# Performance work log

Hardware: AMD Instinct MI355X
Metric: run time of the kernel (lower is better)

## Reference

```python
import jax, jax.numpy as jnp
import numpy as np

B, N, HIDDEN = 1024, 64, 1152
NUM_CLASSES = 1000
OUT_DIM = 4 * 4 * 8  # patch_size^2 * out_channels = 128


def setup_inputs() -> dict:
    key = jax.random.key(0)
    k_x, k_y, k_w = jax.random.split(key, 3)
    x = jax.random.normal(k_x, (B, N, HIDDEN), dtype=jnp.float32)
    y = jax.random.randint(k_y, (B,), 0, NUM_CLASSES, dtype=jnp.int64)
    weight = 0.02 * jax.random.normal(k_w, (NUM_CLASSES, HIDDEN, OUT_DIM), dtype=jnp.float32)
    bias = jnp.zeros((NUM_CLASSES, OUT_DIM), dtype=jnp.float32)
    return {"x": x, "y": y, "weight": weight, "bias": bias}


def reference(x, y, weight, bias):
    # Gather per-sample class weight [B, hidden, out_dim] and bias [B, out_dim],
    # then batched matmul + bias add: [B, N, hidden] @ [B, hidden, out_dim]
    w = weight[y]                      # [B, hidden, out_dim]
    b = bias[y][:, None, :]            # [B, 1, out_dim]
    return jnp.einsum('bnh,bho->bno', x, w) + b
```

## Files before the change

kernel.cpp:

```cpp
#include <hip/hip_runtime.h>


constexpr int Bn = 1024;
constexpr int Nn = 64;
constexpr int Kn = 1152;
constexpr int On = 128;
constexpr int KB = 32;
constexpr int NTHREADS = 128;

__global__ __launch_bounds__(NTHREADS, 2)
void ada_gemm_f32(const float* __restrict__ x,
                  const int* __restrict__ y,
                  const float* __restrict__ w,
                  const float* __restrict__ bias,
                  float* __restrict__ out)
{
    __shared__ float As[Nn][KB + 1];
    __shared__ float Bs[KB][On];

    const int b   = blockIdx.x;
    const int tid = threadIdx.x;
    const int cls = y[b];

    const float* __restrict__ xb = x + (size_t)b * Nn * Kn;
    const float* __restrict__ wb = w + (size_t)cls * Kn * On;

    const int rg = tid >> 4;
    const int cg = tid & 15;
    const int r0 = rg * 8;
    const int c0 = cg * 4;

    float acc[8][8];
    #pragma unroll
    for (int i = 0; i < 8; ++i)
        #pragma unroll
        for (int j = 0; j < 8; ++j)
            acc[i][j] = 0.0f;

    for (int k0 = 0; k0 < Kn; k0 += KB) {
        #pragma unroll
        for (int i = 0; i < 4; ++i) {
            const int f  = tid + i * NTHREADS;
            const int n  = f >> 3;
            const int k4 = f & 7;
            const float4 v = *reinterpret_cast<const float4*>(xb + n * Kn + k0 + k4 * 4);
            As[n][k4 * 4 + 0] = v.x;
            As[n][k4 * 4 + 1] = v.y;
            As[n][k4 * 4 + 2] = v.z;
            As[n][k4 * 4 + 3] = v.w;
        }
        #pragma unroll
        for (int i = 0; i < 8; ++i) {
            const int f  = tid + i * NTHREADS;
            const int kr = f >> 5;
            const int c4 = f & 31;
            const float4 v = *reinterpret_cast<const float4*>(wb + (size_t)(k0 + kr) * On + c4 * 4);
            *reinterpret_cast<float4*>(&Bs[kr][c4 * 4]) = v;
        }
        __syncthreads();

        #pragma unroll
        for (int k = 0; k < KB; ++k) {
            float a[8];
            #pragma unroll
            for (int i = 0; i < 8; ++i)
                a[i] = As[r0 + i][k];
            const float4 b0 = *reinterpret_cast<const float4*>(&Bs[k][c0]);
            const float4 b1 = *reinterpret_cast<const float4*>(&Bs[k][c0 + 64]);
            const float bb[8] = {b0.x, b0.y, b0.z, b0.w, b1.x, b1.y, b1.z, b1.w};
            #pragma unroll
            for (int i = 0; i < 8; ++i)
                #pragma unroll
                for (int j = 0; j < 8; ++j)
                    acc[i][j] = fmaf(a[i], bb[j], acc[i][j]);
        }
        __syncthreads();
    }

    const float4 bi0 = *reinterpret_cast<const float4*>(bias + (size_t)cls * On + c0);
    const float4 bi1 = *reinterpret_cast<const float4*>(bias + (size_t)cls * On + c0 + 64);
    float* __restrict__ ob = out + (size_t)b * Nn * On;
    #pragma unroll
    for (int i = 0; i < 8; ++i) {
        float4 o0, o1;
        o0.x = acc[i][0] + bi0.x;
        o0.y = acc[i][1] + bi0.y;
        o0.z = acc[i][2] + bi0.z;
        o0.w = acc[i][3] + bi0.w;
        o1.x = acc[i][4] + bi1.x;
        o1.y = acc[i][5] + bi1.y;
        o1.z = acc[i][6] + bi1.z;
        o1.w = acc[i][7] + bi1.w;
        *reinterpret_cast<float4*>(ob + (r0 + i) * On + c0)      = o0;
        *reinterpret_cast<float4*>(ob + (r0 + i) * On + c0 + 64) = o1;
    }
}

extern "C" void kernel_launch(void* const* d_in, const int* in_sizes, int n_in,
                              void* d_out, int out_size, void* d_ws, size_t ws_size,
                              hipStream_t stream) {
    const float* x    = (const float*)d_in[0];
    const int*   y    = (const int*)d_in[1];
    const float* w    = (const float*)d_in[2];
    const float* bias = (const float*)d_in[3];
    float* out = (float*)d_out;

    ada_gemm_f32<<<dim3(Bn), dim3(NTHREADS), 0, stream>>>(x, y, w, bias, out);
}
```

Baseline: 979.3 us.

## Use split-bf16 MFMA GEMM with class-sorted block order and register prefetch

Replaces the FP32 FMA tiled GEMM with bf16 MFMA instructions, splitting each float into high and low bf16 parts and using three MFMAs per tile so accuracy stays close to FP32. A small pre-kernel counting-sorts samples by class so that blocks sharing a weight matrix run next to each other and reuse it from cache. Global loads for the next K tile are prefetched into registers while the current tile is computed. The cost is the extra split/convert work, transposed shared-memory stores for B, an extra kernel launch, and a slightly larger rounding error than pure FP32.

```diff
diff --git a/kernel.cpp b/kernel.cpp
--- a/kernel.cpp
+++ b/kernel.cpp
@@ -1,98 +1,181 @@
 #include <hip/hip_runtime.h>
 
+
+typedef __bf16 bf16x8 __attribute__((ext_vector_type(8)));
+typedef float f32x4 __attribute__((ext_vector_type(4)));
 
 constexpr int Bn = 1024;
 constexpr int Nn = 64;
 constexpr int Kn = 1152;
 constexpr int On = 128;
 constexpr int KB = 32;
-constexpr int NTHREADS = 128;
+constexpr int NT = 256;
+constexpr int NTILES = Kn / KB;
+constexpr int RS = 36;
 
-__global__ __launch_bounds__(NTHREADS, 2)
-void ada_gemm_f32(const float* __restrict__ x,
-                  const int* __restrict__ y,
-                  const float* __restrict__ w,
-                  const float* __restrict__ bias,
-                  float* __restrict__ out)
-{
-    __shared__ float As[Nn][KB + 1];
-    __shared__ float Bs[KB][On];
+union FragU {
+    bf16x8 v;
+    uint2 u[2];
+};
+static_assert(sizeof(FragU) == 16, "frag size");
 
-    const int b   = blockIdx.x;
+__device__ __forceinline__ void split2(float f, ushort& hi, ushort& lo) {
+    uint u = __float_as_uint(f);
+    hi = (ushort)(u >> 16);
+    float fl = f - __uint_as_float(u & 0xFFFF0000u);
+    lo = (ushort)(__float_as_uint(fl) >> 16);
+}
+
+__device__ __forceinline__ uint pack2(ushort a, ushort b) {
+    return (uint)a | ((uint)b << 16);
+}
+
+__global__ void sort_classes(const int* __restrict__ y, int* __restrict__ perm) {
+    __shared__ int hist[1024];
+    __shared__ int scan[1024];
+    const int t = threadIdx.x;
+    hist[t] = 0;
+    __syncthreads();
+    const int cls = y[t];
+    atomicAdd(&hist[cls], 1);
+    __syncthreads();
+    const int v = hist[t];
+    scan[t] = v;
+    __syncthreads();
+    for (int off = 1; off < 1024; off <<= 1) {
+        int u = (t >= off) ? scan[t - off] : 0;
+        __syncthreads();
+        scan[t] += u;
+        __syncthreads();
+    }
+    hist[t] = scan[t] - v;
+    __syncthreads();
+    const int pos = atomicAdd(&hist[cls], 1);
+    perm[pos] = t;
+}
+
+__global__ __launch_bounds__(NT, 3)
+void ada_gemm_bf16s(const float* __restrict__ x, const int* __restrict__ y,
+                    const float* __restrict__ w, const float* __restrict__ bias,
+                    const int* __restrict__ perm, float* __restrict__ out) {
+    __shared__ ushort As[2][Nn][RS];
+    __shared__ ushort Bs[2][On][RS];
+
     const int tid = threadIdx.x;
+    const int b   = perm[blockIdx.x];
     const int cls = y[b];
-
     const float* __restrict__ xb = x + (size_t)b * Nn * Kn;
     const float* __restrict__ wb = w + (size_t)cls * Kn * On;
 
-    const int rg = tid >> 4;
-    const int cg = tid & 15;
-    const int r0 = rg * 8;
-    const int c0 = cg * 4;
+    const int lane = tid & 63;
+    const int wid  = tid >> 6;
+    const int wr   = wid >> 1;
+    const int wc   = wid & 1;
+    const int l15  = lane & 15;
+    const int kg   = lane >> 4;
 
-    float acc[8][8];
+    const int an  = tid >> 3;
+    const int ak4 = tid & 7;
+    const int bkr = tid >> 5;
+    const int bo4 = (tid & 31) * 4;
+
+    f32x4 acc[2][4];
     #pragma unroll
-    for (int i = 0; i < 8; ++i)
+    for (int m = 0; m < 2; ++m)
         #pragma unroll
-        for (int j = 0; j < 8; ++j)
-            acc[i][j] = 0.0f;
+        for (int n = 0; n < 4; ++n)
+            acc[m][n] = (f32x4)(0.0f);
 
-    for (int k0 = 0; k0 < Kn; k0 += KB) {
+    float4 pa[2], pb[4];
+    #pragma unroll
+    for (int i = 0; i < 2; ++i)
+        pa[i] = *reinterpret_cast<const float4*>(xb + (size_t)(an + 32 * i) * Kn + ak4 * 4);
+    #pragma unroll
+    for (int i = 0; i < 4; ++i)
+        pb[i] = *reinterpret_cast<const float4*>(wb + (size_t)(bkr + 8 * i) * On + bo4);
+
+    for (int t = 0; t < NTILES; ++t) {
+        __syncthreads();
+
+        #pragma unroll
+        for (int i = 0; i < 2; ++i) {
+            ushort h[4], l[4];
+            split2(pa[i].x, h[0], l[0]);
+            split2(pa[i].y, h[1], l[1]);
+            split2(pa[i].z, h[2], l[2]);
+            split2(pa[i].w, h[3], l[3]);
+            uint2 ph; ph.x = pack2(h[0], h[1]); ph.y = pack2(h[2], h[3]);
+            uint2 pl; pl.x = pack2(l[0], l[1]); pl.y = pack2(l[2], l[3]);
+            *reinterpret_cast<uint2*>(&As[0][an + 32 * i][ak4 * 4]) = ph;
+            *reinterpret_cast<uint2*>(&As[1][an + 32 * i][ak4 * 4]) = pl;
+        }
         #pragma unroll
         for (int i = 0; i < 4; ++i) {
-            const int f  = tid + i * NTHREADS;
-            const int n  = f >> 3;
-            const int k4 = f & 7;
-            const float4 v = *reinterpret_cast<const float4*>(xb + n * Kn + k0 + k4 * 4);
-            As[n][k4 * 4 + 0] = v.x;
-            As[n][k4 * 4 + 1] = v.y;
-            As[n][k4 * 4 + 2] = v.z;
-            As[n][k4 * 4 + 3] = v.w;
+            ushort h[4], l[4];
+            split2(pb[i].x, h[0], l[0]);
+            split2(pb[i].y, h[1], l[1]);
+            split2(pb[i].z, h[2], l[2]);
+            split2(pb[i].w, h[3], l[3]);
+            const int kr = bkr + 8 * i;
+            #pragma unroll
+            for (int j = 0; j < 4; ++j) {
+                Bs[0][bo4 + j][kr] = h[j];
+                Bs[1][bo4 + j][kr] = l[j];
+            }
         }
-        #pragma unroll
-        for (int i = 0; i < 8; ++i) {
-            const int f  = tid + i * NTHREADS;
-            const int kr = f >> 5;
-            const int c4 = f & 31;
-            const float4 v = *reinterpret_cast<const float4*>(wb + (size_t)(k0 + kr) * On + c4 * 4);
-            *reinterpret_cast<float4*>(&Bs[kr][c4 * 4]) = v;
+        if (t + 1 < NTILES) {
+            const int k0 = (t + 1) * KB;
+            #pragma unroll
+            for (int i = 0; i < 2; ++i)
+                pa[i] = *reinterpret_cast<const float4*>(xb + (size_t)(an + 32 * i) * Kn + k0 + ak4 * 4);
+            #pragma unroll
+            for (int i = 0; i < 4; ++i)
+                pb[i] = *reinterpret_cast<const float4*>(wb + (size_t)(k0 + bkr + 8 * i) * On + bo4);
         }
         __syncthreads();
 
+        FragU a[2][2];
+        FragU bf[2][4];
         #pragma unroll
-        for (int k = 0; k < KB; ++k) {
-            float a[8];
+        for (int m = 0; m < 2; ++m) {
+            const int row = wr * 32 + m * 16 + l15;
+            a[0][m].u[0] = *reinterpret_cast<const uint2*>(&As[0][row][kg * 8]);
+            a[0][m].u[1] = *reinterpret_cast<const uint2*>(&As[0][row][kg * 8 + 4]);
+            a[1][m].u[0] = *reinterpret_cast<const uint2*>(&As[1][row][kg * 8]);
+            a[1][m].u[1] = *reinterpret_cast<const uint2*>(&As[1][row][kg * 8 + 4]);
+        }
+        #pragma unroll
+        for (int n = 0; n < 4; ++n) {
+            const int o = wc * 64 + n * 16 + l15;
+            bf[0][n].u[0] = *reinterpret_cast<const uint2*>(&Bs[0][o][kg * 8]);
+            bf[0][n].u[1] = *reinterpret_cast<const uint2*>(&Bs[0][o][kg * 8 + 4]);
+            bf[1][n].u[0] = *reinterpret_cast<const uint2*>(&Bs[1][o][kg * 8]);
+            bf[1][n].u[1] = *reinterpret_cast<const uint2*>(&Bs[1][o][kg * 8 + 4]);
+        }
+        #pragma unroll
+        for (int m = 0; m < 2; ++m) {
             #pragma unroll
-            for (int i = 0; i < 8; ++i)
-                a[i] = As[r0 + i][k];
-            const float4 b0 = *reinterpret_cast<const float4*>(&Bs[k][c0]);
-            const float4 b1 = *reinterpret_cast<const float4*>(&Bs[k][c0 + 64]);
-            const float bb[8] = {b0.x, b0.y, b0.z, b0.w, b1.x, b1.y, b1.z, b1.w};
-            #pragma unroll
-            for (int i = 0; i < 8; ++i)
-                #pragma unroll
-                for (int j = 0; j < 8; ++j)
-                    acc[i][j] = fmaf(a[i], bb[j], acc[i][j]);
+            for (int n = 0; n < 4; ++n) {
+                acc[m][n] = __builtin_amdgcn_mfma_f32_16x16x32_bf16(a[0][m].v, bf[0][n].v, acc[m][n], 0, 0, 0);
+                acc[m][n] = __builtin_amdgcn_mfma_f32_16x16x32_bf16(a[1][m].v, bf[0][n].v, acc[m][n], 0, 0, 0);
+                acc[m][n] = __builtin_amdgcn_mfma_f32_16x16x32_bf16(a[0][m].v, bf[1][n].v, acc[m][n], 0, 0, 0);
+            }
         }
-        __syncthreads();
     }
 
-    const float4 bi0 = *reinterpret_cast<const float4*>(bias + (size_t)cls * On + c0);
-    const float4 bi1 = *reinterpret_cast<const float4*>(bias + (size_t)cls * On + c0 + 64);
     float* __restrict__ ob = out + (size_t)b * Nn * On;
+    const float* __restrict__ bb = bias + (size_t)cls * On;
     #pragma unroll
-    for (int i = 0; i < 8; ++i) {
-        float4 o0, o1;
-        o0.x = acc[i][0] + bi0.x;
-        o0.y = acc[i][1] + bi0.y;
-        o0.z = acc[i][2] + bi0.z;
-        o0.w = acc[i][3] + bi0.w;
-        o1.x = acc[i][4] + bi1.x;
-        o1.y = acc[i][5] + bi1.y;
-        o1.z = acc[i][6] + bi1.z;
-        o1.w = acc[i][7] + bi1.w;
-        *reinterpret_cast<float4*>(ob + (r0 + i) * On + c0)      = o0;
-        *reinterpret_cast<float4*>(ob + (r0 + i) * On + c0 + 64) = o1;
+    for (int n = 0; n < 4; ++n) {
+        const int col = wc * 64 + n * 16 + l15;
+        const float bv = bb[col];
+        #pragma unroll
+        for (int m = 0; m < 2; ++m) {
+            const int row0 = wr * 32 + m * 16 + kg * 4;
+            #pragma unroll
+            for (int r = 0; r < 4; ++r)
+                ob[(size_t)(row0 + r) * On + col] = acc[m][n][r] + bv;
+        }
     }
 }
 
@@ -104,6 +187,8 @@
     const float* w    = (const float*)d_in[2];
     const float* bias = (const float*)d_in[3];
     float* out = (float*)d_out;
+    int* perm  = (int*)d_ws;
 
-    ada_gemm_f32<<<dim3(Bn), dim3(NTHREADS), 0, stream>>>(x, y, w, bias, out);
+    sort_classes<<<dim3(1), dim3(1024), 0, stream>>>(y, perm);
+    ada_gemm_bf16s<<<dim3(Bn), dim3(NT), 0, stream>>>(x, y, w, bias, perm, out);
 }
```

Result: faster. 934.3 us (-4.6%).
